# Kernel optimization log

Measured on AMD Instinct MI355X. Metric: run time of the kernel, lower is better.

The kernel has to match this reference:

```python
import jax, jax.numpy as jnp
import numpy as np
from jax import lax

B, T, D, U, M = 64, 800, 3, 400, 20


def _lstm_peephole(x, Wx, Wh, b, p_i, p_f, p_o):
    """Peephole LSTM over [B,T,Din] -> [B,T,U]. Gate order: i,f,c,o."""
    xW = jnp.einsum('btd,dg->btg', x, Wx) + b  # precompute input projection [B,T,4U]
    h0 = jnp.zeros((x.shape[0], U), x.dtype)
    c0 = jnp.zeros((x.shape[0], U), x.dtype)

    def step(carry, xt):
        h, c = carry
        z = xt + h @ Wh
        zi, zf, zc, zo = jnp.split(z, 4, axis=-1)
        i = jax.nn.sigmoid(zi + p_i * c)
        f = jax.nn.sigmoid(zf + p_f * c)
        c_new = f * c + i * jnp.tanh(zc)
        o = jax.nn.sigmoid(zo + p_o * c_new)
        h_new = o * jnp.tanh(c_new)
        return (h_new, c_new), h_new

    _, hs = lax.scan(step, (h0, c0), jnp.swapaxes(xW, 0, 1))  # [T,B,U]
    return jnp.swapaxes(hs, 0, 1)


def _mdn(h, Wmdn, bmdn):
    y = h @ Wmdn + bmdn  # [B,T,6M+1]
    pi = jax.nn.softmax(y[..., :M], axis=-1)
    mu1 = y[..., M:2 * M]
    mu2 = y[..., 2 * M:3 * M]
    s1 = jnp.exp(y[..., 3 * M:4 * M])
    s2 = jnp.exp(y[..., 4 * M:5 * M])
    rho = jnp.tanh(y[..., 5 * M:6 * M])
    eos = jax.nn.sigmoid(y[..., 6 * M:])
    return jnp.concatenate([pi, mu1, mu2, s1, s2, rho, eos], axis=-1)


def setup_inputs() -> dict:
    key = jax.random.key(0)
    ks = jax.random.split(key, 32)
    s = 0.08
    inp = {'x': jax.random.normal(ks[0], (B, T, D), jnp.float32)}
    k = 1
    for l in range(3):
        din = D if l == 0 else D + U
        inp[f'Wx{l}'] = jax.random.normal(ks[k], (din, 4 * U), jnp.float32) * s; k += 1
        inp[f'Wh{l}'] = jax.random.normal(ks[k], (U, 4 * U), jnp.float32) * s; k += 1
        inp[f'b{l}'] = jnp.zeros((4 * U,), jnp.float32)
        inp[f'peep_i{l}'] = jax.random.normal(ks[k], (U,), jnp.float32) * s; k += 1
        inp[f'peep_f{l}'] = jax.random.normal(ks[k], (U,), jnp.float32) * s; k += 1
        inp[f'peep_o{l}'] = jax.random.normal(ks[k], (U,), jnp.float32) * s; k += 1
    inp['Wmdn'] = jax.random.normal(ks[k], (U, 6 * M + 1), jnp.float32) * s
    inp['bmdn'] = jnp.zeros((6 * M + 1,), jnp.float32)
    return inp


def reference(x, Wx0, Wh0, b0, peep_i0, peep_f0, peep_o0,
              Wx1, Wh1, b1, peep_i1, peep_f1, peep_o1,
              Wx2, Wh2, b2, peep_i2, peep_f2, peep_o2,
              Wmdn, bmdn):
    h = _lstm_peephole(x, Wx0, Wh0, b0, peep_i0, peep_f0, peep_o0)
    # skip connections: layers 1,2 take concat([inputs, prev_hidden])
    h = _lstm_peephole(jnp.concatenate([x, h], axis=-1), Wx1, Wh1, b1, peep_i1, peep_f1, peep_o1)
    h = _lstm_peephole(jnp.concatenate([x, h], axis=-1), Wx2, Wh2, b2, peep_i2, peep_f2, peep_o2)
    return _mdn(h, Wmdn, bmdn)
```

## Files before the change

kernel.cpp:

```cpp
#include <hip/hip_runtime.h>


#define TSTEPS 800
#define NG 4
#define GB 16
#define NSL 5
#define UB 80
#define CB 320
#define KP 416
#define RD 16
#define HXD 4
#define AS 424
#define ZS 332

typedef __attribute__((ext_vector_type(8))) __bf16 bf16x8;
typedef __attribute__((ext_vector_type(4))) float floatx4;

struct Peeps { const float* pi[3]; const float* pf[3]; const float* po[3]; };

__device__ __forceinline__ unsigned short f2bf(float f) {
    unsigned int u = __float_as_uint(f);
    return (unsigned short)((u + 0x7FFFu + ((u >> 16) & 1u)) >> 16);
}
__device__ __forceinline__ float bf_lo(unsigned u) { return __uint_as_float(u << 16); }
__device__ __forceinline__ float bf_hi(unsigned u) { return __uint_as_float(u & 0xFFFF0000u); }
__device__ __forceinline__ float sigm_(float v) { return 1.f / (1.f + __expf(-v)); }
__device__ __forceinline__ float tanh_(float v) { float e = __expf(2.f * v); return 1.f - 2.f / (e + 1.f); }
__device__ __forceinline__ unsigned ld_a(const unsigned* p) {
    return __hip_atomic_load(p, __ATOMIC_RELAXED, __HIP_MEMORY_SCOPE_AGENT);
}
__device__ __forceinline__ void st_a(unsigned* p, unsigned v) {
    __hip_atomic_store(p, v, __ATOMIC_RELAXED, __HIP_MEMORY_SCOPE_AGENT);
}

__global__ void pack_rec(const float* __restrict__ Wx, const float* __restrict__ Wh,
                         const float* __restrict__ bias, unsigned short* __restrict__ dst,
                         int is_l0) {
    int idx = blockIdx.x * 256 + threadIdx.x;
    if (idx >= 1600 * KP) return;
    int col = idx / KP, k = idx - col * KP;
    int co = (col & 3) * 400 + (col >> 2);
    float v = 0.f;
    if (k < 400) v = Wh[k * 1600 + co];
    else if (is_l0) {
        if (k < 403) v = Wx[(k - 400) * 1600 + co];
        else if (k == 403) v = bias[co];
    }
    dst[idx] = f2bf(v);
}
__global__ void pack_pre(const float* __restrict__ Wx, const float* __restrict__ bias,
                         unsigned short* __restrict__ dst) {
    int idx = blockIdx.x * 256 + threadIdx.x;
    if (idx >= 1600 * KP) return;
    int col = idx / KP, k = idx - col * KP;
    int co = (col & 3) * 400 + (col >> 2);
    float v = 0.f;
    if (k < 400) v = Wx[(3 + k) * 1600 + co];
    else if (k < 403) v = Wx[(k - 400) * 1600 + co];
    else if (k == 403) v = bias[co];
    dst[idx] = f2bf(v);
}
__global__ void pack_x(const float* __restrict__ x, unsigned short* __restrict__ xp) {
    int idx = blockIdx.x * 256 + threadIdx.x;
    if (idx >= TSTEPS * 64) return;
    int t = idx / 64, b = idx - t * 64;
    unsigned short o[4];
    for (int d = 0; d < 3; ++d) o[d] = f2bf(x[(b * TSTEPS + t) * 3 + d]);
    o[3] = 0x3F80u;
    *(uint2*)(xp + (size_t)idx * 4) = *(uint2*)o;
}
__global__ void pack_mdn(const float* __restrict__ Wm, const float* __restrict__ bm,
                         unsigned short* __restrict__ dst) {
    int idx = blockIdx.x * 256 + threadIdx.x;
    if (idx >= 128 * KP) return;
    int col = idx / KP, k = idx - col * KP;
    float v = 0.f;
    if (col < 121) {
        if (k < 400) v = Wm[k * 121 + col];
        else if (k == 400) v = bm[col];
    }
    dst[idx] = f2bf(v);
}

__global__ __launch_bounds__(640)
void fused_scan(const unsigned short* __restrict__ Bp,
                const unsigned short* __restrict__ Bpre,
                const unsigned short* __restrict__ xpack,
                unsigned* __restrict__ hx,
                unsigned* __restrict__ hring,
                unsigned* __restrict__ zin,
                unsigned* __restrict__ seqb,
                unsigned* __restrict__ h2,
                Peeps pp) {
    const int tid = threadIdx.x;
    const int lane = tid & 63;
    const int w = tid >> 6;
    const int bid = blockIdx.x;

    __shared__ unsigned short A[32 * AS];
    __shared__ float Z[16 * ZS];

    for (int i = tid; i < 32 * AS; i += 640) A[i] = 0;

    const int er = tid / 40;
    const int up = tid - er * 40;
    const int aoff = (lane & 15) * AS + ((lane >> 4) << 3);
    const int zc0 = w * 32 + (lane & 15);
    const int zr = (lane >> 4) << 2;

    if (bid < 60) {
        const int l = bid / 20;
        const int g = (bid % 20) / 5;
        const int s = bid % 5;
        bf16x8 breg[2][13];
        #pragma unroll
        for (int n = 0; n < 2; ++n) {
            const unsigned short* bpp = Bp + (size_t)l * 1600 * KP
                + (size_t)(s * CB + w * 32 + n * 16 + (lane & 15)) * KP + ((lane >> 4) << 3);
            #pragma unroll
            for (int kt = 0; kt < 13; ++kt) breg[n][kt] = *(const bf16x8*)(bpp + kt * 32);
        }
        unsigned* hxL = hx + (size_t)(l * NG + g) * HXD * 6400;
        unsigned* ringL = hring + (size_t)(l * NG + g) * RD * 3200;
        const unsigned* zinL = zin + (size_t)((l - 1) * NG + g) * RD * 12800;
        unsigned* FHown = seqb + ((l * NG + g) * NSL + s) * 16;
        const unsigned* FZup = seqb + (60 + ((l - 1) * NG + g) * NSL) * 16;
        const unsigned* FZdn = seqb + (60 + (l * NG + g) * NSL) * 16;

        const int p0 = ((s + 1) % 5) * 80, p1 = ((s + 2) % 5) * 80;
        const int p2 = ((s + 3) % 5) * 80, p3 = ((s + 4) % 5) * 80;
        const int ug0 = s * UB + 2 * up;
        const float pi0 = pp.pi[l][ug0], pi1 = pp.pi[l][ug0 + 1];
        const float pf0 = pp.pf[l][ug0], pf1 = pp.pf[l][ug0 + 1];
        const float po0 = pp.po[l][ug0], po1 = pp.po[l][ug0 + 1];
        float c0 = 0.f, c1 = 0.f;

        __syncthreads();
        if (l == 0 && tid < 16)
            *(uint2*)(&A[tid * AS + 400]) = *(const uint2*)(xpack + ((size_t)0 * 64 + g * 16 + tid) * 4);
        __syncthreads();

        for (int t = 0; t < TSTEPS; ++t) {
            {
                const unsigned want = (unsigned)(t - 1) << 16;
                const unsigned* hb = hxL + (size_t)((t + 3) & 3) * 6400 + er * 400 + 2 * up;
                const unsigned* fp = nullptr; unsigned fneed = 0;
                if (l > 0 && (t & 3) == 0 && tid < NSL) { fp = FZup + tid * 16; fneed = (unsigned)(t + 4); }
                else if (l < 2 && (t & 7) == 0 && tid >= NSL && tid < 2 * NSL) {
                    fp = FZdn + (tid - NSL) * 16; fneed = (unsigned)(t > 8 ? t - 8 : 0);
                }
                unsigned v0, v1, v2, v3, v4, v5, v6, v7;
                for (;;) {
                    bool ok = true;
                    if (t > 0) {
                        v0 = ld_a(hb + p0); v1 = ld_a(hb + p0 + 1);
                        v2 = ld_a(hb + p1); v3 = ld_a(hb + p1 + 1);
                        v4 = ld_a(hb + p2); v5 = ld_a(hb + p2 + 1);
                        v6 = ld_a(hb + p3); v7 = ld_a(hb + p3 + 1);
                        ok = ((v0 & 0xFFFF0000u) == want) & ((v1 & 0xFFFF0000u) == want) &
                             ((v2 & 0xFFFF0000u) == want) & ((v3 & 0xFFFF0000u) == want) &
                             ((v4 & 0xFFFF0000u) == want) & ((v5 & 0xFFFF0000u) == want) &
                             ((v6 & 0xFFFF0000u) == want) & ((v7 & 0xFFFF0000u) == want);
                    }
                    if (fp) ok &= (ld_a(fp) >= fneed);
                    if (__all(ok)) break;
                }
                if (t > 0) {
                    const int ab = er * AS + 2 * up;
                    *(unsigned*)&A[ab + p0] = (v0 & 0xFFFFu) | (v1 << 16);
                    *(unsigned*)&A[ab + p1] = (v2 & 0xFFFFu) | (v3 << 16);
                    *(unsigned*)&A[ab + p2] = (v4 & 0xFFFFu) | (v5 << 16);
                    *(unsigned*)&A[ab + p3] = (v6 & 0xFFFFu) | (v7 << 16);
                }
            }
            __syncthreads();
            if (tid == 0) st_a(FHown, (unsigned)t);

            unsigned q0, q1, q2, q3;
            if (l > 0) {
                const unsigned* zp = zinL + (size_t)(t & 15) * 12800 + er * 800 + 4 * (s * 40 + up);
                q0 = ld_a(zp); q1 = ld_a(zp + 1); q2 = ld_a(zp + 2); q3 = ld_a(zp + 3);
            }

            floatx4 a0 = {0, 0, 0, 0}, a1 = {0, 0, 0, 0};
            #pragma unroll
            for (int kt = 0; kt < 13; ++kt) {
                bf16x8 a = *(const bf16x8*)(&A[aoff + kt * 32]);
                a0 = __builtin_amdgcn_mfma_f32_16x16x32_bf16(a, breg[0][kt], a0, 0, 0, 0);
                a1 = __builtin_amdgcn_mfma_f32_16x16x32_bf16(a, breg[1][kt], a1, 0, 0, 0);
            }
            #pragma unroll
            for (int ri = 0; ri < 4; ++ri) {
                Z[(zr + ri) * ZS + zc0] = a0[ri];
                Z[(zr + ri) * ZS + zc0 + 16] = a1[ri];
            }
            __syncthreads();

            float4 za = *(const float4*)(&Z[er * ZS + 8 * up]);
            float4 zb4 = *(const float4*)(&Z[er * ZS + 8 * up + 4]);
            if (l > 0) {
                za.x += bf_lo(q0); za.y += bf_hi(q0); za.z += bf_lo(q1); za.w += bf_hi(q1);
                zb4.x += bf_lo(q2); zb4.y += bf_hi(q2); zb4.z += bf_lo(q3); zb4.w += bf_hi(q3);
            }
            float iv = sigm_(za.x + pi0 * c0);
            float fv = sigm_(za.y + pf0 * c0);
            float cn = fv * c0 + iv * tanh_(za.z);
            float ov = sigm_(za.w + po0 * cn);
            float h0 = ov * tanh_(cn);
            c0 = cn;
            iv = sigm_(zb4.x + pi1 * c1);
            fv = sigm_(zb4.y + pf1 * c1);
            cn = fv * c1 + iv * tanh_(zb4.z);
            ov = sigm_(zb4.w + po1 * cn);
            float h1 = ov * tanh_(cn);
            c1 = cn;
            unsigned packh = (unsigned)f2bf(h0) | ((unsigned)f2bf(h1) << 16);
            *(unsigned*)&A[er * AS + ug0] = packh;
            if (l == 0 && tid < 16 && t + 1 < TSTEPS)
                *(uint2*)(&A[tid * AS + 400]) = *(const uint2*)(xpack + ((size_t)(t + 1) * 64 + g * 16 + tid) * 4);
            __syncthreads();

            unsigned* hxs = hxL + (size_t)(t & 3) * 6400 + er * 400 + ug0;
            st_a(hxs, ((unsigned)t << 16) | (packh & 0xFFFFu));
            st_a(hxs + 1, ((unsigned)t << 16) | (packh >> 16));
            if (l < 2)
                st_a(ringL + (size_t)(t & 15) * 3200 + er * 200 + s * 40 + up, packh);
            else
                h2[(size_t)t * 12800 + (g * GB + er) * 200 + s * 40 + up] = packh;
        }
        __syncthreads();
        if (tid == 0) st_a(FHown, (unsigned)TSTEPS);
    } else {
        const int p = bid - 60;
        const int lz = p / 20;
        const int g = (p % 20) / 5;
        const int sp = p % 5;
        bf16x8 breg[2][13];
        #pragma unroll
        for (int n = 0; n < 2; ++n) {
            const unsigned short* bpp = Bpre + (size_t)lz * 1600 * KP
                + (size_t)(sp * CB + w * 32 + n * 16 + (lane & 15)) * KP + ((lane >> 4) << 3);
            #pragma unroll
            for (int kt = 0; kt < 13; ++kt) breg[n][kt] = *(const bf16x8*)(bpp + kt * 32);
        }
        const unsigned* ringS = hring + (size_t)(lz * NG + g) * RD * 3200;
        unsigned* zinD = zin + (size_t)(lz * NG + g) * RD * 12800;
        const unsigned* FHup = seqb + ((lz * NG + g) * NSL) * 16;
        const unsigned* FHdn = seqb + (((lz + 1) * NG + g) * NSL) * 16;
        unsigned* FZown = seqb + (60 + (lz * NG + g) * NSL + sp) * 16;
        __syncthreads();

        for (int c = 0; c < TSTEPS; c += 2) {
            {
                const unsigned* fp = nullptr; unsigned need = 0;
                if (tid < NSL) { fp = FHup + tid * 16; need = (unsigned)(c + 2); }
                else if (tid < 2 * NSL) { fp = FHdn + (tid - NSL) * 16; need = (unsigned)(c > 14 ? c - 14 : 0); }
                bool ok = (fp == nullptr) || (ld_a(fp) >= need);
                while (!__all(ok)) { if (!ok) ok = ld_a(fp) >= need; }
            }
            __syncthreads();
            if (tid == 0 && c > 0) st_a(FZown, (unsigned)c);

            for (int i = tid; i < 6400; i += 640) {
                int tc = i / 3200, j = i - tc * 3200;
                unsigned v = ld_a(ringS + (size_t)((c + tc) & 15) * 3200 + j);
                int r = j / 200, d = j - r * 200;
                *(unsigned*)&A[(tc * 16 + r) * AS + 2 * d] = v;
            }
            if (tid < 32) {
                int tc = tid >> 4, r = tid & 15;
                *(uint2*)(&A[(tc * 16 + r) * AS + 400]) =
                    *(const uint2*)(xpack + ((size_t)(c + tc) * 64 + g * 16 + r) * 4);
            }
            __syncthreads();

            floatx4 a00 = {0,0,0,0}, a01 = {0,0,0,0}, a10 = {0,0,0,0}, a11 = {0,0,0,0};
            #pragma unroll
            for (int kt = 0; kt < 13; ++kt) {
                bf16x8 x0 = *(const bf16x8*)(&A[aoff + kt * 32]);
                bf16x8 x1 = *(const bf16x8*)(&A[aoff + 16 * AS + kt * 32]);
                a00 = __builtin_amdgcn_mfma_f32_16x16x32_bf16(x0, breg[0][kt], a00, 0, 0, 0);
                a01 = __builtin_amdgcn_mfma_f32_16x16x32_bf16(x0, breg[1][kt], a01, 0, 0, 0);
                a10 = __builtin_amdgcn_mfma_f32_16x16x32_bf16(x1, breg[0][kt], a10, 0, 0, 0);
                a11 = __builtin_amdgcn_mfma_f32_16x16x32_bf16(x1, breg[1][kt], a11, 0, 0, 0);
            }
            #pragma unroll
            for (int m = 0; m < 2; ++m) {
                #pragma unroll
                for (int ri = 0; ri < 4; ++ri) {
                    Z[(zr + ri) * ZS + zc0] = (m ? a10[ri] : a00[ri]);
                    Z[(zr + ri) * ZS + zc0 + 16] = (m ? a11[ri] : a01[ri]);
                }
                __syncthreads();
                float4 za = *(const float4*)(&Z[er * ZS + 8 * up]);
                float4 zbv = *(const float4*)(&Z[er * ZS + 8 * up + 4]);
                unsigned* zg = zinD + (size_t)((c + m) & 15) * 12800 + er * 800 + sp * 160 + 4 * up;
                st_a(zg,     (unsigned)f2bf(za.x) | ((unsigned)f2bf(za.y) << 16));
                st_a(zg + 1, (unsigned)f2bf(za.z) | ((unsigned)f2bf(za.w) << 16));
                st_a(zg + 2, (unsigned)f2bf(zbv.x) | ((unsigned)f2bf(zbv.y) << 16));
                st_a(zg + 3, (unsigned)f2bf(zbv.z) | ((unsigned)f2bf(zbv.w) << 16));
                __syncthreads();
            }
        }
        __syncthreads();
        if (tid == 0) st_a(FZown, (unsigned)TSTEPS);
    }
}

__global__ __launch_bounds__(256)
void mdn_kernel(const unsigned short* __restrict__ h2,
                const unsigned short* __restrict__ Bm,
                float* __restrict__ out) {
    const int blk = blockIdx.x;
    const int b = blk / 25;
    const int t0 = (blk - b * 25) * 32;
    const int tid = threadIdx.x;
    const int lane = tid & 63;
    const int w = tid >> 6;
    const int m = w & 1, nh = w >> 1;

    __shared__ unsigned short A[32 * 424];
    __shared__ float Z[32 * 132];
    __shared__ float rmax[32], rinv[32];

    for (int i = tid; i < 32 * 424; i += 256) A[i] = 0;
    __syncthreads();
    for (int c = tid; c < 32 * 50; c += 256) {
        int r = c / 50, j = c - r * 50;
        *(bf16x8*)(&A[r * 424 + j * 8]) = *(const bf16x8*)(h2 + (size_t)(t0 + r) * 25600 + b * 400 + j * 8);
    }
    if (tid < 32) A[tid * 424 + 400] = 0x3F80u;
    __syncthreads();

    floatx4 acc[4] = {{0,0,0,0},{0,0,0,0},{0,0,0,0},{0,0,0,0}};
    const int aoff = (m * 16 + (lane & 15)) * 424 + ((lane >> 4) << 3);
    #pragma unroll
    for (int kt = 0; kt < 13; ++kt) {
        bf16x8 a = *(const bf16x8*)(&A[aoff + kt * 32]);
        #pragma unroll
        for (int n = 0; n < 4; ++n) {
            const unsigned short* bp = Bm + (size_t)((nh * 4 + n) * 16 + (lane & 15)) * KP
                                          + ((lane >> 4) << 3) + kt * 32;
            acc[n] = __builtin_amdgcn_mfma_f32_16x16x32_bf16(a, *(const bf16x8*)bp, acc[n], 0, 0, 0);
        }
    }
    #pragma unroll
    for (int n = 0; n < 4; ++n) {
        int zc = (nh * 4 + n) * 16 + (lane & 15);
        int zrow = m * 16 + ((lane >> 4) << 2);
        #pragma unroll
        for (int ri = 0; ri < 4; ++ri)
            Z[(zrow + ri) * 132 + zc] = acc[n][ri];
    }
    __syncthreads();
    if (tid < 32) {
        float mx = -1e30f;
        for (int j = 0; j < 20; ++j) mx = fmaxf(mx, Z[tid * 132 + j]);
        float sm = 0.f;
        for (int j = 0; j < 20; ++j) sm += __expf(Z[tid * 132 + j] - mx);
        rmax[tid] = mx;
        rinv[tid] = 1.f / sm;
    }
    __syncthreads();
    for (int idx = tid; idx < 32 * 121; idx += 256) {
        int r = idx / 121, jo = idx - r * 121;
        float v = Z[r * 132 + jo];
        float o;
        if (jo < 20) o = __expf(v - rmax[r]) * rinv[r];
        else if (jo < 60) o = v;
        else if (jo < 100) o = __expf(v);
        else if (jo < 120) o = tanh_(v);
        else o = sigm_(v);
        out[(size_t)(b * TSTEPS + t0 + r) * 121 + jo] = o;
    }
}

extern "C" void kernel_launch(void* const* d_in, const int* in_sizes, int n_in,
                              void* d_out, int out_size, void* d_ws, size_t ws_size,
                              hipStream_t stream) {
    const float* x = (const float*)d_in[0];
    const float* Wx[3] = {(const float*)d_in[1], (const float*)d_in[7], (const float*)d_in[13]};
    const float* Wh[3] = {(const float*)d_in[2], (const float*)d_in[8], (const float*)d_in[14]};
    const float* bb[3] = {(const float*)d_in[3], (const float*)d_in[9], (const float*)d_in[15]};
    Peeps pp;
    for (int l = 0; l < 3; ++l) {
        pp.pi[l] = (const float*)d_in[4 + 6 * l];
        pp.pf[l] = (const float*)d_in[5 + 6 * l];
        pp.po[l] = (const float*)d_in[6 + 6 * l];
    }
    const float* Wm = (const float*)d_in[19];
    const float* bm = (const float*)d_in[20];
    float* out = (float*)d_out;

    char* base = (char*)d_ws;
    size_t off = 0;
    auto alloc = [&](size_t bytes) -> void* {
        void* r = base + off;
        off = (off + bytes + 255) & ~(size_t)255;
        return r;
    };
    unsigned* seqb        = (unsigned*)alloc(1600 * sizeof(unsigned));
    unsigned* hx          = (unsigned*)alloc((size_t)3 * NG * HXD * 6400 * 4);
    unsigned* hring       = (unsigned*)alloc((size_t)3 * NG * RD * 3200 * 4);
    unsigned* zin         = (unsigned*)alloc((size_t)2 * NG * RD * 12800 * 4);
    unsigned short* Bp    = (unsigned short*)alloc((size_t)3 * 1600 * KP * 2);
    unsigned short* Bpre  = (unsigned short*)alloc((size_t)2 * 1600 * KP * 2);
    unsigned short* Bm    = (unsigned short*)alloc((size_t)128 * KP * 2);
    unsigned short* xpk   = (unsigned short*)alloc((size_t)TSTEPS * 64 * 4 * 2);
    unsigned short* h2    = (unsigned short*)alloc((size_t)TSTEPS * 64 * 400 * 2);

    hipMemsetAsync(seqb, 0, 1600 * sizeof(unsigned), stream);
    hipMemsetAsync(hx, 0xAA, (size_t)3 * NG * HXD * 6400 * 4, stream);

    for (int l = 0; l < 3; ++l)
        pack_rec<<<2600, 256, 0, stream>>>(Wx[l], Wh[l], bb[l], Bp + (size_t)l * 1600 * KP, l == 0);
    pack_pre<<<2600, 256, 0, stream>>>(Wx[1], bb[1], Bpre);
    pack_pre<<<2600, 256, 0, stream>>>(Wx[2], bb[2], Bpre + (size_t)1600 * KP);
    pack_x<<<200, 256, 0, stream>>>(x, xpk);
    pack_mdn<<<208, 256, 0, stream>>>(Wm, bm, Bm);

    fused_scan<<<100, 640, 0, stream>>>(Bp, Bpre, xpk, hx, hring, zin, seqb,
                                        (unsigned*)h2, pp);

    mdn_kernel<<<1600, 256, 0, stream>>>(h2, Bm, out);
}
```

Baseline: 3.034 ms.

## Swap MFMA operands so gates land in registers, drop Z staging and barriers

The recurrent MFMA now puts weights in the A operand and hidden state in the B operand, so each lane's accumulator holds the four gates (i,f,c,o) of one unit for one batch row. This removes the shared-memory Z transpose and one or two __syncthreads per timestep, and the z-projection producer does the same. The hidden-state LDS buffer is double-buffered so the next step's h can be written without a barrier. Cross-slice h packing now uses lane shuffles, and the zin layout changes to unit-major 64-bit reads. This relies on the new zin and ring layouts matching between the producer and consumer blocks, and on the bias column at index 403 being set correctly.

```diff
diff --git a/kernel.cpp b/kernel.cpp
--- a/kernel.cpp
+++ b/kernel.cpp
@@ -11,7 +11,6 @@
 #define RD 16
 #define HXD 4
 #define AS 424
-#define ZS 332
 
 typedef __attribute__((ext_vector_type(8))) __bf16 bf16x8;
 typedef __attribute__((ext_vector_type(4))) float floatx4;
@@ -27,6 +26,9 @@
 __device__ __forceinline__ float sigm_(float v) { return 1.f / (1.f + __expf(-v)); }
 __device__ __forceinline__ float tanh_(float v) { float e = __expf(2.f * v); return 1.f - 2.f / (e + 1.f); }
 __device__ __forceinline__ unsigned ld_a(const unsigned* p) {
+    return __hip_atomic_load(p, __ATOMIC_RELAXED, __HIP_MEMORY_SCOPE_AGENT);
+}
+__device__ __forceinline__ unsigned long long ld_a64(const unsigned long long* p) {
     return __hip_atomic_load(p, __ATOMIC_RELAXED, __HIP_MEMORY_SCOPE_AGENT);
 }
 __device__ __forceinline__ void st_a(unsigned* p, unsigned v) {
@@ -97,16 +99,15 @@
     const int w = tid >> 6;
     const int bid = blockIdx.x;
 
-    __shared__ unsigned short A[32 * AS];
-    __shared__ float Z[16 * ZS];
-
-    for (int i = tid; i < 32 * AS; i += 640) A[i] = 0;
+    __shared__ unsigned short A[2 * 16 * AS];
+
+    for (int i = tid; i < 2 * 16 * AS; i += 640) A[i] = 0;
 
     const int er = tid / 40;
     const int up = tid - er * 40;
     const int aoff = (lane & 15) * AS + ((lane >> 4) << 3);
-    const int zc0 = w * 32 + (lane & 15);
-    const int zr = (lane >> 4) << 2;
+    const int b = lane & 15;
+    const int q = lane >> 4;
 
     if (bid < 60) {
         const int l = bid / 20;
@@ -116,31 +117,35 @@
         #pragma unroll
         for (int n = 0; n < 2; ++n) {
             const unsigned short* bpp = Bp + (size_t)l * 1600 * KP
-                + (size_t)(s * CB + w * 32 + n * 16 + (lane & 15)) * KP + ((lane >> 4) << 3);
+                + (size_t)(s * CB + w * 32 + n * 16 + b) * KP + (q << 3);
             #pragma unroll
             for (int kt = 0; kt < 13; ++kt) breg[n][kt] = *(const bf16x8*)(bpp + kt * 32);
         }
         unsigned* hxL = hx + (size_t)(l * NG + g) * HXD * 6400;
         unsigned* ringL = hring + (size_t)(l * NG + g) * RD * 3200;
-        const unsigned* zinL = zin + (size_t)((l - 1) * NG + g) * RD * 12800;
+        const unsigned long long* zinL =
+            (const unsigned long long*)(zin + (size_t)((l - 1) * NG + g) * RD * 12800);
         unsigned* FHown = seqb + ((l * NG + g) * NSL + s) * 16;
         const unsigned* FZup = seqb + (60 + ((l - 1) * NG + g) * NSL) * 16;
         const unsigned* FZdn = seqb + (60 + (l * NG + g) * NSL) * 16;
 
         const int p0 = ((s + 1) % 5) * 80, p1 = ((s + 2) % 5) * 80;
         const int p2 = ((s + 3) % 5) * 80, p3 = ((s + 4) % 5) * 80;
-        const int ug0 = s * UB + 2 * up;
-        const float pi0 = pp.pi[l][ug0], pi1 = pp.pi[l][ug0 + 1];
-        const float pf0 = pp.pf[l][ug0], pf1 = pp.pf[l][ug0 + 1];
-        const float po0 = pp.po[l][ug0], po1 = pp.po[l][ug0 + 1];
-        float c0 = 0.f, c1 = 0.f;
+        const int ugA = s * UB + w * 8 + q;
+        const int ugB = ugA + 4;
+        const float piA = pp.pi[l][ugA], pfA = pp.pf[l][ugA], poA = pp.po[l][ugA];
+        const float piB = pp.pi[l][ugB], pfB = pp.pf[l][ugB], poB = pp.po[l][ugB];
+        float cA = 0.f, cB = 0.f;
 
         __syncthreads();
-        if (l == 0 && tid < 16)
-            *(uint2*)(&A[tid * AS + 400]) = *(const uint2*)(xpack + ((size_t)0 * 64 + g * 16 + tid) * 4);
+        if (l == 0 && tid < 32) {
+            int bf_ = tid >> 4, r = tid & 15;
+            A[bf_ * 16 * AS + r * AS + 403] = 0x3F80u;
+        }
         __syncthreads();
 
         for (int t = 0; t < TSTEPS; ++t) {
+            unsigned short* bufC = A + (t & 1) * 16 * AS;
             {
                 const unsigned want = (unsigned)(t - 1) << 16;
                 const unsigned* hb = hxL + (size_t)((t + 3) & 3) * 6400 + er * 400 + 2 * up;
@@ -167,66 +172,80 @@
                 }
                 if (t > 0) {
                     const int ab = er * AS + 2 * up;
-                    *(unsigned*)&A[ab + p0] = (v0 & 0xFFFFu) | (v1 << 16);
-                    *(unsigned*)&A[ab + p1] = (v2 & 0xFFFFu) | (v3 << 16);
-                    *(unsigned*)&A[ab + p2] = (v4 & 0xFFFFu) | (v5 << 16);
-                    *(unsigned*)&A[ab + p3] = (v6 & 0xFFFFu) | (v7 << 16);
+                    *(unsigned*)&bufC[ab + p0] = (v0 & 0xFFFFu) | (v1 << 16);
+                    *(unsigned*)&bufC[ab + p1] = (v2 & 0xFFFFu) | (v3 << 16);
+                    *(unsigned*)&bufC[ab + p2] = (v4 & 0xFFFFu) | (v5 << 16);
+                    *(unsigned*)&bufC[ab + p3] = (v6 & 0xFFFFu) | (v7 << 16);
                 }
             }
+            if (l == 0 && tid < 16)
+                *(uint2*)(&bufC[tid * AS + 400]) = *(const uint2*)(xpack + ((size_t)t * 64 + g * 16 + tid) * 4);
             __syncthreads();
             if (tid == 0) st_a(FHown, (unsigned)t);
 
-            unsigned q0, q1, q2, q3;
+            unsigned long long zuA = 0, zuB = 0;
             if (l > 0) {
-                const unsigned* zp = zinL + (size_t)(t & 15) * 12800 + er * 800 + 4 * (s * 40 + up);
-                q0 = ld_a(zp); q1 = ld_a(zp + 1); q2 = ld_a(zp + 2); q3 = ld_a(zp + 3);
+                const unsigned long long* zp = zinL + (size_t)(t & 15) * 6400 + b;
+                zuA = ld_a64(zp + ugA * 16);
+                zuB = ld_a64(zp + ugB * 16);
             }
 
             floatx4 a0 = {0, 0, 0, 0}, a1 = {0, 0, 0, 0};
             #pragma unroll
             for (int kt = 0; kt < 13; ++kt) {
-                bf16x8 a = *(const bf16x8*)(&A[aoff + kt * 32]);
-                a0 = __builtin_amdgcn_mfma_f32_16x16x32_bf16(a, breg[0][kt], a0, 0, 0, 0);
-                a1 = __builtin_amdgcn_mfma_f32_16x16x32_bf16(a, breg[1][kt], a1, 0, 0, 0);
-            }
-            #pragma unroll
-            for (int ri = 0; ri < 4; ++ri) {
-                Z[(zr + ri) * ZS + zc0] = a0[ri];
-                Z[(zr + ri) * ZS + zc0 + 16] = a1[ri];
-            }
-            __syncthreads();
-
-            float4 za = *(const float4*)(&Z[er * ZS + 8 * up]);
-            float4 zb4 = *(const float4*)(&Z[er * ZS + 8 * up + 4]);
+                bf16x8 h = *(const bf16x8*)(&bufC[aoff + kt * 32]);
+                a0 = __builtin_amdgcn_mfma_f32_16x16x32_bf16(breg[0][kt], h, a0, 0, 0, 0);
+                a1 = __builtin_amdgcn_mfma_f32_16x16x32_bf16(breg[1][kt], h, a1, 0, 0, 0);
+            }
+
+            float zi = a0[0], zf = a0[1], zc = a0[2], zo = a0[3];
             if (l > 0) {
-                za.x += bf_lo(q0); za.y += bf_hi(q0); za.z += bf_lo(q1); za.w += bf_hi(q1);
-                zb4.x += bf_lo(q2); zb4.y += bf_hi(q2); zb4.z += bf_lo(q3); zb4.w += bf_hi(q3);
-            }
-            float iv = sigm_(za.x + pi0 * c0);
-            float fv = sigm_(za.y + pf0 * c0);
-            float cn = fv * c0 + iv * tanh_(za.z);
-            float ov = sigm_(za.w + po0 * cn);
+                unsigned lo = (unsigned)zuA, hi = (unsigned)(zuA >> 32);
+                zi += bf_lo(lo); zf += bf_hi(lo); zc += bf_lo(hi); zo += bf_hi(hi);
+            }
+            float iv = sigm_(zi + piA * cA);
+            float fv = sigm_(zf + pfA * cA);
+            float cn = fv * cA + iv * tanh_(zc);
+            float ov = sigm_(zo + poA * cn);
             float h0 = ov * tanh_(cn);
-            c0 = cn;
-            iv = sigm_(zb4.x + pi1 * c1);
-            fv = sigm_(zb4.y + pf1 * c1);
-            cn = fv * c1 + iv * tanh_(zb4.z);
-            ov = sigm_(zb4.w + po1 * cn);
+            cA = cn;
+            zi = a1[0]; zf = a1[1]; zc = a1[2]; zo = a1[3];
+            if (l > 0) {
+                unsigned lo = (unsigned)zuB, hi = (unsigned)(zuB >> 32);
+                zi += bf_lo(lo); zf += bf_hi(lo); zc += bf_lo(hi); zo += bf_hi(hi);
+            }
+            iv = sigm_(zi + piB * cB);
+            fv = sigm_(zf + pfB * cB);
+            cn = fv * cB + iv * tanh_(zc);
+            ov = sigm_(zo + poB * cn);
             float h1 = ov * tanh_(cn);
-            c1 = cn;
-            unsigned packh = (unsigned)f2bf(h0) | ((unsigned)f2bf(h1) << 16);
-            *(unsigned*)&A[er * AS + ug0] = packh;
-            if (l == 0 && tid < 16 && t + 1 < TSTEPS)
-                *(uint2*)(&A[tid * AS + 400]) = *(const uint2*)(xpack + ((size_t)(t + 1) * 64 + g * 16 + tid) * 4);
-            __syncthreads();
-
-            unsigned* hxs = hxL + (size_t)(t & 3) * 6400 + er * 400 + ug0;
-            st_a(hxs, ((unsigned)t << 16) | (packh & 0xFFFFu));
-            st_a(hxs + 1, ((unsigned)t << 16) | (packh >> 16));
-            if (l < 2)
-                st_a(ringL + (size_t)(t & 15) * 3200 + er * 200 + s * 40 + up, packh);
-            else
-                h2[(size_t)t * 12800 + (g * GB + er) * 200 + s * 40 + up] = packh;
+            cB = cn;
+
+            unsigned hu0 = f2bf(h0), hu1 = f2bf(h1);
+            unsigned short* bufN = A + ((t + 1) & 1) * 16 * AS;
+            bufN[b * AS + ugA] = (unsigned short)hu0;
+            bufN[b * AS + ugB] = (unsigned short)hu1;
+
+            unsigned* hxs = hxL + (size_t)(t & 3) * 6400 + b * 400;
+            st_a(hxs + ugA, ((unsigned)t << 16) | hu0);
+            st_a(hxs + ugB, ((unsigned)t << 16) | hu1);
+
+            unsigned r0 = (unsigned)__shfl_xor((int)hu0, 16);
+            unsigned r1 = (unsigned)__shfl_xor((int)hu1, 16);
+            if (!(q & 1)) {
+                unsigned pk0 = hu0 | (r0 << 16);
+                unsigned pk1 = hu1 | (r1 << 16);
+                int di = b * 200 + s * 40 + w * 4 + (q >> 1);
+                if (l < 2) {
+                    unsigned* rg = ringL + (size_t)(t & 15) * 3200;
+                    st_a(rg + di, pk0);
+                    st_a(rg + di + 2, pk1);
+                } else {
+                    unsigned* hg = h2 + (size_t)t * 12800 + (size_t)g * GB * 200;
+                    hg[di] = pk0;
+                    hg[di + 2] = pk1;
+                }
+            }
         }
         __syncthreads();
         if (tid == 0) st_a(FHown, (unsigned)TSTEPS);
@@ -239,7 +258,7 @@
         #pragma unroll
         for (int n = 0; n < 2; ++n) {
             const unsigned short* bpp = Bpre + (size_t)lz * 1600 * KP
-                + (size_t)(sp * CB + w * 32 + n * 16 + (lane & 15)) * KP + ((lane >> 4) << 3);
+                + (size_t)(sp * CB + w * 32 + n * 16 + b) * KP + (q << 3);
             #pragma unroll
             for (int kt = 0; kt < 13; ++kt) breg[n][kt] = *(const bf16x8*)(bpp + kt * 32);
         }
@@ -248,6 +267,8 @@
         const unsigned* FHup = seqb + ((lz * NG + g) * NSL) * 16;
         const unsigned* FHdn = seqb + (((lz + 1) * NG + g) * NSL) * 16;
         unsigned* FZown = seqb + (60 + (lz * NG + g) * NSL + sp) * 16;
+        const int uA = sp * UB + w * 8 + q;
+        const int uB = uA + 4;
         __syncthreads();
 
         for (int c = 0; c < TSTEPS; c += 2) {
@@ -279,27 +300,23 @@
             for (int kt = 0; kt < 13; ++kt) {
                 bf16x8 x0 = *(const bf16x8*)(&A[aoff + kt * 32]);
                 bf16x8 x1 = *(const bf16x8*)(&A[aoff + 16 * AS + kt * 32]);
-                a00 = __builtin_amdgcn_mfma_f32_16x16x32_bf16(x0, breg[0][kt], a00, 0, 0, 0);
-                a01 = __builtin_amdgcn_mfma_f32_16x16x32_bf16(x0, breg[1][kt], a01, 0, 0, 0);
-                a10 = __builtin_amdgcn_mfma_f32_16x16x32_bf16(x1, breg[0][kt], a10, 0, 0, 0);
-                a11 = __builtin_amdgcn_mfma_f32_16x16x32_bf16(x1, breg[1][kt], a11, 0, 0, 0);
-            }
-            #pragma unroll
-            for (int m = 0; m < 2; ++m) {
-                #pragma unroll
-                for (int ri = 0; ri < 4; ++ri) {
-                    Z[(zr + ri) * ZS + zc0] = (m ? a10[ri] : a00[ri]);
-                    Z[(zr + ri) * ZS + zc0 + 16] = (m ? a11[ri] : a01[ri]);
-                }
-                __syncthreads();
-                float4 za = *(const float4*)(&Z[er * ZS + 8 * up]);
-                float4 zbv = *(const float4*)(&Z[er * ZS + 8 * up + 4]);
-                unsigned* zg = zinD + (size_t)((c + m) & 15) * 12800 + er * 800 + sp * 160 + 4 * up;
-                st_a(zg,     (unsigned)f2bf(za.x) | ((unsigned)f2bf(za.y) << 16));
-                st_a(zg + 1, (unsigned)f2bf(za.z) | ((unsigned)f2bf(za.w) << 16));
-                st_a(zg + 2, (unsigned)f2bf(zbv.x) | ((unsigned)f2bf(zbv.y) << 16));
-                st_a(zg + 3, (unsigned)f2bf(zbv.z) | ((unsigned)f2bf(zbv.w) << 16));
-                __syncthreads();
+                a00 = __builtin_amdgcn_mfma_f32_16x16x32_bf16(breg[0][kt], x0, a00, 0, 0, 0);
+                a01 = __builtin_amdgcn_mfma_f32_16x16x32_bf16(breg[1][kt], x0, a01, 0, 0, 0);
+                a10 = __builtin_amdgcn_mfma_f32_16x16x32_bf16(breg[0][kt], x1, a10, 0, 0, 0);
+                a11 = __builtin_amdgcn_mfma_f32_16x16x32_bf16(breg[1][kt], x1, a11, 0, 0, 0);
+            }
+            {
+                unsigned* z0 = zinD + (size_t)(c & 15) * 12800;
+                unsigned* z1 = zinD + (size_t)((c + 1) & 15) * 12800;
+                int iA = (uA * 16 + b) * 2, iB = (uB * 16 + b) * 2;
+                st_a(z0 + iA,     (unsigned)f2bf(a00[0]) | ((unsigned)f2bf(a00[1]) << 16));
+                st_a(z0 + iA + 1, (unsigned)f2bf(a00[2]) | ((unsigned)f2bf(a00[3]) << 16));
+                st_a(z0 + iB,     (unsigned)f2bf(a01[0]) | ((unsigned)f2bf(a01[1]) << 16));
+                st_a(z0 + iB + 1, (unsigned)f2bf(a01[2]) | ((unsigned)f2bf(a01[3]) << 16));
+                st_a(z1 + iA,     (unsigned)f2bf(a10[0]) | ((unsigned)f2bf(a10[1]) << 16));
+                st_a(z1 + iA + 1, (unsigned)f2bf(a10[2]) | ((unsigned)f2bf(a10[3]) << 16));
+                st_a(z1 + iB,     (unsigned)f2bf(a11[0]) | ((unsigned)f2bf(a11[1]) << 16));
+                st_a(z1 + iB + 1, (unsigned)f2bf(a11[2]) | ((unsigned)f2bf(a11[3]) << 16));
             }
         }
         __syncthreads();
@@ -312,8 +329,8 @@
                 const unsigned short* __restrict__ Bm,
                 float* __restrict__ out) {
     const int blk = blockIdx.x;
-    const int b = blk / 25;
-    const int t0 = (blk - b * 25) * 32;
+    const int bb = blk / 25;
+    const int t0 = (blk - bb * 25) * 32;
     const int tid = threadIdx.x;
     const int lane = tid & 63;
     const int w = tid >> 6;
@@ -327,7 +344,7 @@
     __syncthreads();
     for (int c = tid; c < 32 * 50; c += 256) {
         int r = c / 50, j = c - r * 50;
-        *(bf16x8*)(&A[r * 424 + j * 8]) = *(const bf16x8*)(h2 + (size_t)(t0 + r) * 25600 + b * 400 + j * 8);
+        *(bf16x8*)(&A[r * 424 + j * 8]) = *(const bf16x8*)(h2 + (size_t)(t0 + r) * 25600 + bb * 400 + j * 8);
     }
     if (tid < 32) A[tid * 424 + 400] = 0x3F80u;
     __syncthreads();
@@ -371,7 +388,7 @@
         else if (jo < 100) o = __expf(v);
         else if (jo < 120) o = tanh_(v);
         else o = sigm_(v);
-        out[(size_t)(b * TSTEPS + t0 + r) * 121 + jo] = o;
+        out[(size_t)(bb * TSTEPS + t0 + r) * 121 + jo] = o;
     }
 }
 
```

New measurement: 3.839 ms. +26.5%, slower.
